# Performance work log

Hardware: AMD Instinct MI355X
Metric: run time of the kernel (lower is better)

The kernel has to match this reference:

```python
import jax, jax.numpy as jnp
import numpy as np

D_MODEL = 1024
D_HIDDEN = 4096
N_EXPERTS = 8
B, S = 2, 2048


def setup_inputs() -> dict:
    key = jax.random.key(0)
    ks = jax.random.split(key, 4)
    sd = 1.0 / np.sqrt(D_MODEL)
    sh = 1.0 / np.sqrt(D_HIDDEN)
    return {
        "x": jax.random.normal(ks[0], (B, S, D_MODEL), dtype=jnp.float32),
        "Wg": jax.random.normal(ks[1], (D_MODEL, N_EXPERTS), dtype=jnp.float32) * sd,
        "bg": jnp.zeros((N_EXPERTS,), dtype=jnp.float32),
        "W1": jax.random.normal(ks[2], (N_EXPERTS, D_MODEL, D_HIDDEN), dtype=jnp.float32) * sd,
        "b1": jnp.zeros((N_EXPERTS, D_HIDDEN), dtype=jnp.float32),
        "W2": jax.random.normal(ks[3], (N_EXPERTS, D_HIDDEN, D_MODEL), dtype=jnp.float32) * sh,
        "b2": jnp.zeros((N_EXPERTS, D_MODEL), dtype=jnp.float32),
    }


def reference(x, Wg, bg, W1, b1, W2, b2):
    # Router: softmax is monotone, so argmax(softmax(logits)) == argmax(logits).
    logits = jnp.einsum("bsd,de->bse", x, Wg) + bg
    expert_idx = jnp.argmax(logits, axis=-1)  # [B, S]
    # Top-1 dispatch, expressed as compute-all-experts + per-token select
    # (jit-friendly; the torch loop masks/gathers per expert).
    h = jax.nn.gelu(jnp.einsum("bsd,edh->bseh", x, W1) + b1, approximate=False)
    y = jnp.einsum("bseh,ehd->bsed", h, W2) + b2  # [B, S, E, D]
    out = jnp.take_along_axis(y, expert_idx[:, :, None, None], axis=2)[:, :, 0, :]
    return out
```

## Files before the change

### kernel.cpp

```cpp
#include <hip/hip_runtime.h>
#include <hip/hip_bf16.h>
#include <math.h>

#define D_MODEL 1024
#define D_HIDDEN 4096
#define N_EXP 8
#define N_TOK 4096

typedef __attribute__((ext_vector_type(8))) __bf16 bf16x8_t;
typedef __attribute__((ext_vector_type(4))) float f32x4_t;

#define WS_BUCKET_OFF 256
#define WS_XB_OFF     (1u << 18)
#define WS_H_OFF      ((1u << 18) + (8u << 20))

__device__ __forceinline__ void gload16(const void* g, void* l) {
    __builtin_amdgcn_global_load_lds(
        (__attribute__((address_space(1))) void*)(g),
        (__attribute__((address_space(3))) void*)(l),
        16, 0, 0);
}

__global__ __launch_bounds__(64) void init_counts(int* counts) {
    if (threadIdx.x < N_EXP) counts[threadIdx.x] = 0;
}

__global__ __launch_bounds__(256) void router_kernel(
    const float* __restrict__ x, const float* __restrict__ Wg,
    const float* __restrict__ bg, int* __restrict__ counts,
    int* __restrict__ bucket, __hip_bfloat16* __restrict__ xb)
{
    const int wid  = threadIdx.x >> 6;
    const int lane = threadIdx.x & 63;
    const int t    = blockIdx.x * 4 + wid;
    const float* xr = x + (size_t)t * D_MODEL;

    double acc[N_EXP];
#pragma unroll
    for (int e = 0; e < N_EXP; ++e) acc[e] = 0.0;

#pragma unroll
    for (int j = 0; j < D_MODEL / 64; ++j) {
        const int d = j * 64 + lane;
        const float xv = xr[d];
        xb[(size_t)t * D_MODEL + d] = __float2bfloat16(xv);
        const float4* wr = (const float4*)(Wg + (size_t)d * N_EXP);
        const float4 w0 = wr[0], w1 = wr[1];
        const double xd = (double)xv;
        acc[0] += xd * (double)w0.x; acc[1] += xd * (double)w0.y;
        acc[2] += xd * (double)w0.z; acc[3] += xd * (double)w0.w;
        acc[4] += xd * (double)w1.x; acc[5] += xd * (double)w1.y;
        acc[6] += xd * (double)w1.z; acc[7] += xd * (double)w1.w;
    }
#pragma unroll
    for (int e = 0; e < N_EXP; ++e) {
        double v = acc[e];
#pragma unroll
        for (int off = 32; off >= 1; off >>= 1) v += __shfl_xor(v, off, 64);
        acc[e] = v + (double)bg[e];
    }
    if (lane == 0) {
        int best = 0; double bv = acc[0];
#pragma unroll
        for (int e = 1; e < N_EXP; ++e)
            if (acc[e] > bv) { bv = acc[e]; best = e; }
        const int pos = atomicAdd(&counts[best], 1);
        bucket[best * N_TOK + pos] = t;
    }
}

template<int K_TOT, int N_TOT, bool IS_FFN1>
__global__ __launch_bounds__(256) void ffn_gemm(
    const __hip_bfloat16* __restrict__ A,
    const float* __restrict__ W,
    const float* __restrict__ bias,
    const int* __restrict__ counts,
    const int* __restrict__ bucket,
    __hip_bfloat16* __restrict__ hout,
    float* __restrict__ yout)
{
    const int e   = blockIdx.z;
    const int cnt = counts[e];
    const int m0  = blockIdx.y * 64;
    if (m0 >= cnt) return;
    const int n0   = blockIdx.x * 64;
    const int tid  = threadIdx.x;
    const int lane = tid & 63;
    const int wid  = tid >> 6;
    const int wm   = wid >> 1, wn = wid & 1;

    __shared__ __hip_bfloat16 As[64 * 64];
    __shared__ __hip_bfloat16 Bs[64 * 64];
    __shared__ int s_tok[64];

    if (tid < 64) {
        int idx = m0 + tid;
        if (idx >= cnt) idx = cnt - 1;
        s_tok[tid] = bucket[e * N_TOK + idx];
    }
    __syncthreads();

    const int rA0 = wid * 16 + (lane >> 3);
    const int rA1 = rA0 + 8;
    const int tok0 = s_tok[rA0];
    const int tok1 = s_tok[rA1];
    const __hip_bfloat16* ga0 = A + (size_t)tok0 * K_TOT + (((lane & 7) ^ (rA0 & 7)) << 3);
    const __hip_bfloat16* ga1 = A + (size_t)tok1 * K_TOT + (((lane & 7) ^ (rA1 & 7)) << 3);
    char* lbA0 = (char*)As + (wid * 16) * 128;
    char* lbA1 = (char*)As + (wid * 16 + 8) * 128;

    const int bc  = tid & 15;
    const int bkq = tid >> 4;
    const float* wbase = W + (size_t)e * K_TOT * N_TOT + (size_t)(bkq * 4) * N_TOT + n0 + bc * 4;

    f32x4_t acc[2][2];
#pragma unroll
    for (int f = 0; f < 2; ++f)
#pragma unroll
        for (int g = 0; g < 2; ++g) acc[f][g] = (f32x4_t){0.f, 0.f, 0.f, 0.f};

#pragma unroll 2
    for (int k0 = 0; k0 < K_TOT; k0 += 64) {
        gload16(ga0 + k0, lbA0);
        gload16(ga1 + k0, lbA1);
        const float* wk = wbase + (size_t)k0 * N_TOT;
        const float4 v0 = *(const float4*)(wk + 0 * (size_t)N_TOT);
        const float4 v1 = *(const float4*)(wk + 1 * (size_t)N_TOT);
        const float4 v2 = *(const float4*)(wk + 2 * (size_t)N_TOT);
        const float4 v3 = *(const float4*)(wk + 3 * (size_t)N_TOT);
#pragma unroll
        for (int i = 0; i < 4; ++i) {
            const int n = bc * 4 + i;
            union { __hip_bfloat16 hh[4]; unsigned long long u; } pk;
            pk.hh[0] = __float2bfloat16(((const float*)&v0)[i]);
            pk.hh[1] = __float2bfloat16(((const float*)&v1)[i]);
            pk.hh[2] = __float2bfloat16(((const float*)&v2)[i]);
            pk.hh[3] = __float2bfloat16(((const float*)&v3)[i]);
            const int phys = n * 128 + (((bkq >> 1) ^ (n & 7)) << 4) + ((bkq & 1) << 3);
            *(unsigned long long*)((char*)Bs + phys) = pk.u;
        }
        __syncthreads();

#pragma unroll
        for (int kk = 0; kk < 2; ++kk) {
            uint4 af[2], bfr[2];
            const int ks = kk * 4 + (lane >> 4);
#pragma unroll
            for (int f = 0; f < 2; ++f) {
                const int r = wm * 32 + f * 16 + (lane & 15);
                af[f] = *(const uint4*)((const char*)As + r * 128 + ((ks ^ (r & 7)) << 4));
            }
#pragma unroll
            for (int g = 0; g < 2; ++g) {
                const int n = wn * 32 + g * 16 + (lane & 15);
                bfr[g] = *(const uint4*)((const char*)Bs + n * 128 + ((ks ^ (n & 7)) << 4));
            }
#pragma unroll
            for (int f = 0; f < 2; ++f)
#pragma unroll
                for (int g = 0; g < 2; ++g)
                    acc[f][g] = __builtin_amdgcn_mfma_f32_16x16x32_bf16(
                        __builtin_bit_cast(bf16x8_t, af[f]),
                        __builtin_bit_cast(bf16x8_t, bfr[g]),
                        acc[f][g], 0, 0, 0);
        }
        __syncthreads();
    }

#pragma unroll
    for (int f = 0; f < 2; ++f) {
#pragma unroll
        for (int j = 0; j < 4; ++j) {
            const int rl = wm * 32 + f * 16 + (lane >> 4) * 4 + j;
            const bool ok = (m0 + rl) < cnt;
            const int tok = s_tok[rl];
#pragma unroll
            for (int g = 0; g < 2; ++g) {
                const int col = n0 + wn * 32 + g * 16 + (lane & 15);
                float v = acc[f][g][j] + bias[e * N_TOT + col];
                if (IS_FFN1) {
                    v = 0.5f * v * (1.0f + erff(v * 0.70710678118654752f));
                    if (ok) hout[(size_t)tok * N_TOT + col] = __float2bfloat16(v);
                } else {
                    if (ok) yout[(size_t)tok * N_TOT + col] = v;
                }
            }
        }
    }
}

extern "C" void kernel_launch(void* const* d_in, const int* in_sizes, int n_in,
                              void* d_out, int out_size, void* d_ws, size_t ws_size,
                              hipStream_t stream) {
    const float* x  = (const float*)d_in[0];
    const float* Wg = (const float*)d_in[1];
    const float* bg = (const float*)d_in[2];
    const float* W1 = (const float*)d_in[3];
    const float* b1 = (const float*)d_in[4];
    const float* W2 = (const float*)d_in[5];
    const float* b2 = (const float*)d_in[6];
    float* out = (float*)d_out;

    char* ws = (char*)d_ws;
    int* counts = (int*)(ws);
    int* bucket = (int*)(ws + WS_BUCKET_OFF);
    __hip_bfloat16* xb = (__hip_bfloat16*)(ws + WS_XB_OFF);
    __hip_bfloat16* h  = (__hip_bfloat16*)(ws + WS_H_OFF);

    init_counts<<<dim3(1), dim3(64), 0, stream>>>(counts);
    router_kernel<<<dim3(N_TOK / 4), dim3(256), 0, stream>>>(x, Wg, bg, counts, bucket, xb);
    ffn_gemm<D_MODEL, D_HIDDEN, true><<<dim3(D_HIDDEN / 64, N_TOK / 64, N_EXP), dim3(256), 0, stream>>>(
        xb, W1, b1, counts, bucket, h, nullptr);
    ffn_gemm<D_HIDDEN, D_MODEL, false><<<dim3(D_MODEL / 64, N_TOK / 64, N_EXP), dim3(256), 0, stream>>>(
        h, W2, b2, counts, bucket, nullptr, out);
}
```

Measured before the change: 337.2 us.

## Enlarge grouped FFN GEMM tiles to 128x128 with 4x4 MFMA per warp

Grows the per-block output tile from 64x64 to 128x128, so each warp now computes a 64x64 sub-tile with a 4x4 grid of MFMA accumulators. The aim is to cut redundant global loads of the fp32 expert weights and the gathered bf16 activations and raise arithmetic intensity per LDS stage. The B-tile staging is reorganised so each thread converts 8 k-rows into one 16-byte LDS store, with a rotated write order to spread bank conflicts. In exchange, register pressure rises (launch bounds now request 2 blocks per CU), fewer blocks run, and ragged per-expert token counts waste more of each tile.

Result: slower. 964.4 us (+186.0%).

```diff
diff --git a/kernel.cpp b/kernel.cpp
--- a/kernel.cpp
+++ b/kernel.cpp
@@ -70,7 +70,7 @@
 }
 
 template<int K_TOT, int N_TOT, bool IS_FFN1>
-__global__ __launch_bounds__(256) void ffn_gemm(
+__global__ __launch_bounds__(256, 2) void ffn_gemm(
     const __hip_bfloat16* __restrict__ A,
     const float* __restrict__ W,
     const float* __restrict__ bias,
@@ -81,102 +81,100 @@
 {
     const int e   = blockIdx.z;
     const int cnt = counts[e];
-    const int m0  = blockIdx.y * 64;
+    const int m0  = blockIdx.y * 128;
     if (m0 >= cnt) return;
-    const int n0   = blockIdx.x * 64;
+    const int n0   = blockIdx.x * 128;
     const int tid  = threadIdx.x;
     const int lane = tid & 63;
     const int wid  = tid >> 6;
     const int wm   = wid >> 1, wn = wid & 1;
 
-    __shared__ __hip_bfloat16 As[64 * 64];
-    __shared__ __hip_bfloat16 Bs[64 * 64];
-    __shared__ int s_tok[64];
-
-    if (tid < 64) {
+    __shared__ __hip_bfloat16 As[128 * 64];
+    __shared__ __hip_bfloat16 Bs[128 * 64];
+    __shared__ int s_tok[128];
+
+    if (tid < 128) {
         int idx = m0 + tid;
         if (idx >= cnt) idx = cnt - 1;
         s_tok[tid] = bucket[e * N_TOK + idx];
     }
     __syncthreads();
 
-    const int rA0 = wid * 16 + (lane >> 3);
-    const int rA1 = rA0 + 8;
-    const int tok0 = s_tok[rA0];
-    const int tok1 = s_tok[rA1];
-    const __hip_bfloat16* ga0 = A + (size_t)tok0 * K_TOT + (((lane & 7) ^ (rA0 & 7)) << 3);
-    const __hip_bfloat16* ga1 = A + (size_t)tok1 * K_TOT + (((lane & 7) ^ (rA1 & 7)) << 3);
-    char* lbA0 = (char*)As + (wid * 16) * 128;
-    char* lbA1 = (char*)As + (wid * 16 + 8) * 128;
-
-    const int bc  = tid & 15;
-    const int bkq = tid >> 4;
-    const float* wbase = W + (size_t)e * K_TOT * N_TOT + (size_t)(bkq * 4) * N_TOT + n0 + bc * 4;
-
-    f32x4_t acc[2][2];
-#pragma unroll
-    for (int f = 0; f < 2; ++f)
-#pragma unroll
-        for (int g = 0; g < 2; ++g) acc[f][g] = (f32x4_t){0.f, 0.f, 0.f, 0.f};
-
-#pragma unroll 2
+    const __hip_bfloat16* gA[4];
+    char* lA[4];
+#pragma unroll
+    for (int i = 0; i < 4; ++i) {
+        const int r = wid * 32 + i * 8 + (lane >> 3);
+        const int tok = s_tok[r];
+        gA[i] = A + (size_t)tok * K_TOT + (((lane & 7) ^ (r & 7)) << 3);
+        lA[i] = (char*)As + (size_t)(wid * 32 + i * 8) * 128;
+    }
+
+    const int bgq = tid & 31;
+    const int bq  = tid >> 5;
+    const float* wb = W + (size_t)e * K_TOT * N_TOT + (size_t)(bq * 8) * N_TOT + n0 + bgq * 4;
+
+    f32x4_t acc[4][4];
+#pragma unroll
+    for (int f = 0; f < 4; ++f)
+#pragma unroll
+        for (int g = 0; g < 4; ++g) acc[f][g] = (f32x4_t){0.f, 0.f, 0.f, 0.f};
+
     for (int k0 = 0; k0 < K_TOT; k0 += 64) {
-        gload16(ga0 + k0, lbA0);
-        gload16(ga1 + k0, lbA1);
-        const float* wk = wbase + (size_t)k0 * N_TOT;
-        const float4 v0 = *(const float4*)(wk + 0 * (size_t)N_TOT);
-        const float4 v1 = *(const float4*)(wk + 1 * (size_t)N_TOT);
-        const float4 v2 = *(const float4*)(wk + 2 * (size_t)N_TOT);
-        const float4 v3 = *(const float4*)(wk + 3 * (size_t)N_TOT);
+#pragma unroll
+        for (int i = 0; i < 4; ++i) gload16(gA[i] + k0, lA[i]);
+
+        const float* wk = wb + (size_t)k0 * N_TOT;
+        float4 v[8];
+#pragma unroll
+        for (int j = 0; j < 8; ++j) v[j] = *(const float4*)(wk + (size_t)j * N_TOT);
 #pragma unroll
         for (int i = 0; i < 4; ++i) {
-            const int n = bc * 4 + i;
-            union { __hip_bfloat16 hh[4]; unsigned long long u; } pk;
-            pk.hh[0] = __float2bfloat16(((const float*)&v0)[i]);
-            pk.hh[1] = __float2bfloat16(((const float*)&v1)[i]);
-            pk.hh[2] = __float2bfloat16(((const float*)&v2)[i]);
-            pk.hh[3] = __float2bfloat16(((const float*)&v3)[i]);
-            const int phys = n * 128 + (((bkq >> 1) ^ (n & 7)) << 4) + ((bkq & 1) << 3);
-            *(unsigned long long*)((char*)Bs + phys) = pk.u;
+            const int ii = (i + bgq) & 3;
+            const int n = bgq * 4 + ii;
+            union { __hip_bfloat16 hh[8]; uint4 u; } pk;
+#pragma unroll
+            for (int j = 0; j < 8; ++j) pk.hh[j] = __float2bfloat16(((const float*)&v[j])[ii]);
+            *(uint4*)((char*)Bs + n * 128 + ((bq ^ (n & 7)) << 4)) = pk.u;
         }
         __syncthreads();
 
 #pragma unroll
         for (int kk = 0; kk < 2; ++kk) {
-            uint4 af[2], bfr[2];
-            const int ks = kk * 4 + (lane >> 4);
-#pragma unroll
-            for (int f = 0; f < 2; ++f) {
-                const int r = wm * 32 + f * 16 + (lane & 15);
-                af[f] = *(const uint4*)((const char*)As + r * 128 + ((ks ^ (r & 7)) << 4));
+            uint4 af[4], bf[4];
+            const int ko = kk * 4 + (lane >> 4);
+#pragma unroll
+            for (int f = 0; f < 4; ++f) {
+                const int r = wm * 64 + f * 16 + (lane & 15);
+                af[f] = *(const uint4*)((const char*)As + r * 128 + ((ko ^ (r & 7)) << 4));
             }
 #pragma unroll
-            for (int g = 0; g < 2; ++g) {
-                const int n = wn * 32 + g * 16 + (lane & 15);
-                bfr[g] = *(const uint4*)((const char*)Bs + n * 128 + ((ks ^ (n & 7)) << 4));
+            for (int g = 0; g < 4; ++g) {
+                const int n = wn * 64 + g * 16 + (lane & 15);
+                bf[g] = *(const uint4*)((const char*)Bs + n * 128 + ((ko ^ (n & 7)) << 4));
             }
 #pragma unroll
-            for (int f = 0; f < 2; ++f)
-#pragma unroll
-                for (int g = 0; g < 2; ++g)
+            for (int f = 0; f < 4; ++f)
+#pragma unroll
+                for (int g = 0; g < 4; ++g)
                     acc[f][g] = __builtin_amdgcn_mfma_f32_16x16x32_bf16(
                         __builtin_bit_cast(bf16x8_t, af[f]),
-                        __builtin_bit_cast(bf16x8_t, bfr[g]),
+                        __builtin_bit_cast(bf16x8_t, bf[g]),
                         acc[f][g], 0, 0, 0);
         }
         __syncthreads();
     }
 
 #pragma unroll
-    for (int f = 0; f < 2; ++f) {
+    for (int f = 0; f < 4; ++f) {
 #pragma unroll
         for (int j = 0; j < 4; ++j) {
-            const int rl = wm * 32 + f * 16 + (lane >> 4) * 4 + j;
+            const int rl = wm * 64 + f * 16 + (lane >> 4) * 4 + j;
             const bool ok = (m0 + rl) < cnt;
             const int tok = s_tok[rl];
 #pragma unroll
-            for (int g = 0; g < 2; ++g) {
-                const int col = n0 + wn * 32 + g * 16 + (lane & 15);
+            for (int g = 0; g < 4; ++g) {
+                const int col = n0 + wn * 64 + g * 16 + (lane & 15);
                 float v = acc[f][g][j] + bias[e * N_TOT + col];
                 if (IS_FFN1) {
                     v = 0.5f * v * (1.0f + erff(v * 0.70710678118654752f));
@@ -209,8 +207,8 @@
 
     init_counts<<<dim3(1), dim3(64), 0, stream>>>(counts);
     router_kernel<<<dim3(N_TOK / 4), dim3(256), 0, stream>>>(x, Wg, bg, counts, bucket, xb);
-    ffn_gemm<D_MODEL, D_HIDDEN, true><<<dim3(D_HIDDEN / 64, N_TOK / 64, N_EXP), dim3(256), 0, stream>>>(
+    ffn_gemm<D_MODEL, D_HIDDEN, true><<<dim3(D_HIDDEN / 128, N_TOK / 128, N_EXP), dim3(256), 0, stream>>>(
         xb, W1, b1, counts, bucket, h, nullptr);
-    ffn_gemm<D_HIDDEN, D_MODEL, false><<<dim3(D_MODEL / 64, N_TOK / 64, N_EXP), dim3(256), 0, stream>>>(
+    ffn_gemm<D_HIDDEN, D_MODEL, false><<<dim3(D_MODEL / 128, N_TOK / 128, N_EXP), dim3(256), 0, stream>>>(
         h, W2, b2, counts, bucket, nullptr, out);
 }
```
